# Kernel optimization log

Measured on AMD Instinct MI355X. Metric: run time of the kernel, lower is better.

Reference implementation:

```python
import jax, jax.numpy as jnp
import numpy as np

N, F_IN, HID, E1, E2, P = 100000, 128, 128, 800000, 800000, 200000


def setup_inputs() -> dict:
    key = jax.random.key(0)
    ks = jax.random.split(key, 9)
    x = jax.random.normal(ks[0], (N, F_IN), dtype=jnp.float32)
    edge_index1 = jax.random.randint(ks[1], (2, E1), 0, N)
    edge_index2 = jax.random.randint(ks[2], (2, E2), 0, N)
    edge_weight1 = jax.random.uniform(ks[3], (E1,), dtype=jnp.float32)
    edge_weight2 = jax.random.uniform(ks[4], (E2,), dtype=jnp.float32)
    pos_edge_index = jax.random.randint(ks[5], (2, P), 0, N)
    # parameters (fan-in scaled init)
    W1 = jax.random.normal(ks[6], (F_IN, HID), dtype=jnp.float32) / np.sqrt(F_IN)
    W2 = jax.random.normal(ks[7], (HID, HID), dtype=jnp.float32) / np.sqrt(HID)
    Wlin = jax.random.normal(ks[8], (2, 2 * HID), dtype=jnp.float32) / np.sqrt(2 * HID)  # torch Linear [out,in]
    return {"x": x, "edge_index1": edge_index1, "edge_index2": edge_index2,
            "edge_weight1": edge_weight1, "edge_weight2": edge_weight2,
            "pos_edge_index": pos_edge_index, "W1": W1, "W2": W2, "Wlin": Wlin}


def gcn_conv(x, W, edge_index, edge_weight, num_nodes):
    # GCNConv(add_self_loops=False, normalize=False, bias=False):
    # out[i] = sum_{(j->i) in E} w_e * (x @ W)[j]
    xw = x @ W                                    # [N, H]
    msg = xw[edge_index[0]] * edge_weight[:, None]  # [E, H] gather + scale
    return jax.ops.segment_sum(msg, edge_index[1], num_segments=num_nodes)


def reference(x, edge_index1, edge_index2, edge_weight1, edge_weight2,
              pos_edge_index, W1, W2, Wlin):
    n = x.shape[0]
    h = jax.nn.relu(gcn_conv(x, W1, edge_index1, edge_weight1, n))
    z = gcn_conv(h, W2, edge_index2, edge_weight2, n)          # [N, H]
    pair = jnp.concatenate([z[pos_edge_index[0]], z[pos_edge_index[1]]], axis=1)  # [P, 2H]
    return pair @ Wlin.T                                        # [P, 2]
```

## Files before the change

### kernel.cpp

```cpp
#include <hip/hip_runtime.h>

#define F 128
#define BSH 9
#define BSZ 512
#define NBLKA 256

typedef __bf16 bf16x8 __attribute__((ext_vector_type(8)));
typedef unsigned short ushort8 __attribute__((ext_vector_type(8)));
typedef unsigned short ushort4v __attribute__((ext_vector_type(4)));
typedef float f32x4 __attribute__((ext_vector_type(4)));

static __device__ __forceinline__ unsigned short f2bf(float f) {
    unsigned int u = __float_as_uint(f);
    u += 0x7fffu + ((u >> 16) & 1u);
    return (unsigned short)(u >> 16);
}
static __device__ __forceinline__ void bf2x(unsigned int u, float& lo, float& hi) {
    lo = __uint_as_float(u << 16);
    hi = __uint_as_float(u & 0xffff0000u);
}

#define WPITCH 136

template <int RELU, int INBF>
__global__ __launch_bounds__(256) void gemm128_mfma(const void* __restrict__ Xv,
                                                    const float* __restrict__ W,
                                                    unsigned short* __restrict__ Y,
                                                    int n) {
    __shared__ __align__(16) unsigned short WT[F * WPITCH];
    for (int idx = threadIdx.x; idx < F * F; idx += 256) {
        const int k = idx >> 7, c = idx & 127;
        WT[c * WPITCH + k] = f2bf(W[idx]);
    }
    __syncthreads();

    const int lane = threadIdx.x & 63;
    const int wv = threadIdx.x >> 6;
    const int m15 = lane & 15;
    const int quad = lane >> 4;
    const int rowBase = blockIdx.x * 128 + wv * 32;

    f32x4 acc[2][8];
#pragma unroll
    for (int rt = 0; rt < 2; ++rt)
#pragma unroll
        for (int ct = 0; ct < 8; ++ct) acc[rt][ct] = (f32x4){0.f, 0.f, 0.f, 0.f};

    int rA[2];
    rA[0] = min(rowBase + m15, n - 1);
    rA[1] = min(rowBase + 16 + m15, n - 1);

#pragma unroll
    for (int ks = 0; ks < 4; ++ks) {
        const int k0 = ks * 32 + quad * 8;
        bf16x8 a[2];
#pragma unroll
        for (int rt = 0; rt < 2; ++rt) {
            if (INBF) {
                const unsigned short* Xb = (const unsigned short*)Xv;
                ushort8 u = *(const ushort8*)(Xb + (size_t)rA[rt] * F + k0);
                if (RELU) {
#pragma unroll
                    for (int j = 0; j < 8; ++j) u[j] = (u[j] & 0x8000u) ? 0 : u[j];
                }
                a[rt] = __builtin_bit_cast(bf16x8, u);
            } else {
                const float* Xf = (const float*)Xv;
                const float* p = Xf + (size_t)rA[rt] * F + k0;
                float4 lo = *(const float4*)p;
                float4 hi = *(const float4*)(p + 4);
                if (RELU) {
                    lo.x = fmaxf(lo.x, 0.f); lo.y = fmaxf(lo.y, 0.f);
                    lo.z = fmaxf(lo.z, 0.f); lo.w = fmaxf(lo.w, 0.f);
                    hi.x = fmaxf(hi.x, 0.f); hi.y = fmaxf(hi.y, 0.f);
                    hi.z = fmaxf(hi.z, 0.f); hi.w = fmaxf(hi.w, 0.f);
                }
                ushort8 u;
                u[0] = f2bf(lo.x); u[1] = f2bf(lo.y); u[2] = f2bf(lo.z); u[3] = f2bf(lo.w);
                u[4] = f2bf(hi.x); u[5] = f2bf(hi.y); u[6] = f2bf(hi.z); u[7] = f2bf(hi.w);
                a[rt] = __builtin_bit_cast(bf16x8, u);
            }
        }
#pragma unroll
        for (int ct = 0; ct < 8; ++ct) {
            const int nn = ct * 16 + m15;
            const bf16x8 b = *(const bf16x8*)(WT + nn * WPITCH + k0);
            acc[0][ct] = __builtin_amdgcn_mfma_f32_16x16x32_bf16(a[0], b, acc[0][ct], 0, 0, 0);
            acc[1][ct] = __builtin_amdgcn_mfma_f32_16x16x32_bf16(a[1], b, acc[1][ct], 0, 0, 0);
        }
    }

#pragma unroll
    for (int rt = 0; rt < 2; ++rt)
#pragma unroll
        for (int reg = 0; reg < 4; ++reg) {
            const int row = rowBase + rt * 16 + quad * 4 + reg;
            if (row < n) {
#pragma unroll
                for (int ct = 0; ct < 8; ++ct)
                    Y[(size_t)row * F + ct * 16 + m15] = f2bf(acc[rt][ct][reg]);
            }
        }
}


__global__ __launch_bounds__(256) void binhist(const int* __restrict__ ei,
                                               int* __restrict__ gh, int E, int nbin) {
    __shared__ int h[1024];
    for (int i = threadIdx.x; i < nbin; i += 256) h[i] = 0;
    __syncthreads();
    const int chunk = (E + NBLKA - 1) / NBLKA;
    const int lo = blockIdx.x * chunk;
    const int hi = min(lo + chunk, E);
    for (int e = lo + threadIdx.x; e < hi; e += 256)
        atomicAdd(&h[((unsigned)ei[E + e]) >> BSH], 1);
    __syncthreads();
    for (int i = threadIdx.x; i < nbin; i += 256) gh[i * NBLKA + blockIdx.x] = h[i];
}

__global__ __launch_bounds__(256) void scan_pass1(const int* __restrict__ counts,
                                                  int* __restrict__ bsum, int n) {
    __shared__ int sh[256];
    const int base = blockIdx.x * 1024 + threadIdx.x * 4;
    int s = 0;
#pragma unroll
    for (int j = 0; j < 4; ++j) {
        const int i = base + j;
        if (i < n) s += counts[i];
    }
    sh[threadIdx.x] = s;
    __syncthreads();
    for (int off = 128; off > 0; off >>= 1) {
        if (threadIdx.x < off) sh[threadIdx.x] += sh[threadIdx.x + off];
        __syncthreads();
    }
    if (threadIdx.x == 0) bsum[blockIdx.x] = sh[0];
}

__global__ __launch_bounds__(256) void scan_pass2(int* __restrict__ bsum, int nb) {
    __shared__ int sh[256];
    int v = (threadIdx.x < nb) ? bsum[threadIdx.x] : 0;
    sh[threadIdx.x] = v;
    __syncthreads();
    for (int off = 1; off < 256; off <<= 1) {
        int t = (threadIdx.x >= off) ? sh[threadIdx.x - off] : 0;
        __syncthreads();
        sh[threadIdx.x] += t;
        __syncthreads();
    }
    if (threadIdx.x < nb) bsum[threadIdx.x] = sh[threadIdx.x] - v;
    if (threadIdx.x == nb) bsum[nb] = sh[nb - 1];
}

__global__ __launch_bounds__(256) void scan_pass3(const int* __restrict__ counts,
                                                  const int* __restrict__ bsum,
                                                  int* __restrict__ offs,
                                                  int n, int nb) {
    __shared__ int sh[256];
    const int base = blockIdx.x * 1024 + threadIdx.x * 4;
    int c[4];
    int s = 0;
#pragma unroll
    for (int j = 0; j < 4; ++j) {
        const int i = base + j;
        c[j] = (i < n) ? counts[i] : 0;
        s += c[j];
    }
    int inc = s;
    sh[threadIdx.x] = inc;
    __syncthreads();
    for (int off = 1; off < 256; off <<= 1) {
        int t = (threadIdx.x >= off) ? sh[threadIdx.x - off] : 0;
        __syncthreads();
        sh[threadIdx.x] += t;
        __syncthreads();
    }
    int run = bsum[blockIdx.x] + sh[threadIdx.x] - inc;
#pragma unroll
    for (int j = 0; j < 4; ++j) {
        const int i = base + j;
        if (i < n) offs[i] = run;
        run += c[j];
    }
    if (blockIdx.x == 0 && threadIdx.x == 0) offs[n] = bsum[nb];
}

__global__ __launch_bounds__(256) void binscatter(const int* __restrict__ ei,
                                                  const float* __restrict__ ew,
                                                  const int* __restrict__ ghoffs,
                                                  uint2* __restrict__ Epart,
                                                  int E, int nbin) {
    __shared__ int gbase[1024];
    __shared__ int cur[1024];
    for (int i = threadIdx.x; i < nbin; i += 256) {
        gbase[i] = ghoffs[i * NBLKA + blockIdx.x];
        cur[i] = 0;
    }
    __syncthreads();
    const int chunk = (E + NBLKA - 1) / NBLKA;
    const int lo = blockIdx.x * chunk;
    const int hi = min(lo + chunk, E);
    for (int e = lo + threadIdx.x; e < hi; e += 256) {
        const unsigned int dst = (unsigned int)ei[E + e];
        const unsigned int src = (unsigned int)ei[e];
        const int b = (int)(dst >> BSH);
        const int r = atomicAdd(&cur[b], 1);
        Epart[(size_t)gbase[b] + r] =
            make_uint2(src | ((dst & (BSZ - 1)) << 20), (unsigned)__float_as_int(ew[e]));
    }
}

__global__ __launch_bounds__(512) void sort_bin(const uint2* __restrict__ Epart,
                                                const int* __restrict__ ghoffs,
                                                uint2* __restrict__ Sedge,
                                                int2* __restrict__ ebounds,
                                                int n, int nbin) {
    __shared__ int hist[BSZ], pref[BSZ], cur[BSZ];
    const int bin = blockIdx.x;
    const int tid = threadIdx.x;
    const int base = ghoffs[bin * NBLKA];
    const int end  = ghoffs[(bin + 1) * NBLKA];
    hist[tid] = 0;
    __syncthreads();
    for (int i = base + tid; i < end; i += 512)
        atomicAdd(&hist[Epart[i].x >> 20], 1);
    __syncthreads();
    pref[tid] = hist[tid];
    __syncthreads();
    for (int off = 1; off < BSZ; off <<= 1) {
        int t = (tid >= off) ? pref[tid - off] : 0;
        __syncthreads();
        pref[tid] += t;
        __syncthreads();
    }
    {
        const int inc = pref[tid];
        const int ex = inc - hist[tid];
        cur[tid] = ex;
        const int v = (bin << BSH) + tid;
        if (v < n) ebounds[v] = make_int2(base + ex, base + inc);
    }
    __syncthreads();
    for (int i = base + tid; i < end; i += 512) {
        const uint2 e = Epart[i];
        const int pos = atomicAdd(&cur[e.x >> 20], 1);
        Sedge[(size_t)base + pos] = make_uint2(e.x & 0xFFFFFu, e.y);
    }
}

template <int FUSE_U>
__global__ __launch_bounds__(256) void gather_agg(const unsigned short* __restrict__ XW,
                                                  const int2* __restrict__ ebounds,
                                                  const uint2* __restrict__ Sedge,
                                                  const float* __restrict__ Wlin,
                                                  unsigned short* __restrict__ OUT,
                                                  float4* __restrict__ U, int n) {
    __shared__ float WL[512];
    if (FUSE_U) {
        for (int i = threadIdx.x; i < 512; i += 256) WL[i] = Wlin[i];
        __syncthreads();
    }
    const int l = threadIdx.x & 15;
    const int v = blockIdx.x * 16 + (threadIdx.x >> 4);
    if (v >= n) return;
    float acc[8];
#pragma unroll
    for (int j = 0; j < 8; ++j) acc[j] = 0.f;
    const int2 be = ebounds[v];
    int p = be.x;
    const int e2 = be.y;
    for (; p + 4 <= e2; p += 4) {
        const uint2 s0 = Sedge[p],     s1 = Sedge[p + 1];
        const uint2 s2 = Sedge[p + 2], s3 = Sedge[p + 3];
        const uint4 x0 = ((const uint4*)(XW + (size_t)s0.x * F))[l];
        const uint4 x1 = ((const uint4*)(XW + (size_t)s1.x * F))[l];
        const uint4 x2 = ((const uint4*)(XW + (size_t)s2.x * F))[l];
        const uint4 x3 = ((const uint4*)(XW + (size_t)s3.x * F))[l];
        const float w0 = __int_as_float(s0.y), w1 = __int_as_float(s1.y);
        const float w2 = __int_as_float(s2.y), w3 = __int_as_float(s3.y);
        float a0, a1, a2, a3, a4, a5, a6, a7;
        bf2x(x0.x, a0, a1); bf2x(x0.y, a2, a3); bf2x(x0.z, a4, a5); bf2x(x0.w, a6, a7);
        acc[0] = fmaf(w0, a0, acc[0]); acc[1] = fmaf(w0, a1, acc[1]);
        acc[2] = fmaf(w0, a2, acc[2]); acc[3] = fmaf(w0, a3, acc[3]);
        acc[4] = fmaf(w0, a4, acc[4]); acc[5] = fmaf(w0, a5, acc[5]);
        acc[6] = fmaf(w0, a6, acc[6]); acc[7] = fmaf(w0, a7, acc[7]);
        bf2x(x1.x, a0, a1); bf2x(x1.y, a2, a3); bf2x(x1.z, a4, a5); bf2x(x1.w, a6, a7);
        acc[0] = fmaf(w1, a0, acc[0]); acc[1] = fmaf(w1, a1, acc[1]);
        acc[2] = fmaf(w1, a2, acc[2]); acc[3] = fmaf(w1, a3, acc[3]);
        acc[4] = fmaf(w1, a4, acc[4]); acc[5] = fmaf(w1, a5, acc[5]);
        acc[6] = fmaf(w1, a6, acc[6]); acc[7] = fmaf(w1, a7, acc[7]);
        bf2x(x2.x, a0, a1); bf2x(x2.y, a2, a3); bf2x(x2.z, a4, a5); bf2x(x2.w, a6, a7);
        acc[0] = fmaf(w2, a0, acc[0]); acc[1] = fmaf(w2, a1, acc[1]);
        acc[2] = fmaf(w2, a2, acc[2]); acc[3] = fmaf(w2, a3, acc[3]);
        acc[4] = fmaf(w2, a4, acc[4]); acc[5] = fmaf(w2, a5, acc[5]);
        acc[6] = fmaf(w2, a6, acc[6]); acc[7] = fmaf(w2, a7, acc[7]);
        bf2x(x3.x, a0, a1); bf2x(x3.y, a2, a3); bf2x(x3.z, a4, a5); bf2x(x3.w, a6, a7);
        acc[0] = fmaf(w3, a0, acc[0]); acc[1] = fmaf(w3, a1, acc[1]);
        acc[2] = fmaf(w3, a2, acc[2]); acc[3] = fmaf(w3, a3, acc[3]);
        acc[4] = fmaf(w3, a4, acc[4]); acc[5] = fmaf(w3, a5, acc[5]);
        acc[6] = fmaf(w3, a6, acc[6]); acc[7] = fmaf(w3, a7, acc[7]);
    }
    for (; p < e2; ++p) {
        const uint2 s = Sedge[p];
        const float w = __int_as_float(s.y);
        const uint4 x = ((const uint4*)(XW + (size_t)s.x * F))[l];
        float a0, a1, a2, a3, a4, a5, a6, a7;
        bf2x(x.x, a0, a1); bf2x(x.y, a2, a3); bf2x(x.z, a4, a5); bf2x(x.w, a6, a7);
        acc[0] = fmaf(w, a0, acc[0]); acc[1] = fmaf(w, a1, acc[1]);
        acc[2] = fmaf(w, a2, acc[2]); acc[3] = fmaf(w, a3, acc[3]);
        acc[4] = fmaf(w, a4, acc[4]); acc[5] = fmaf(w, a5, acc[5]);
        acc[6] = fmaf(w, a6, acc[6]); acc[7] = fmaf(w, a7, acc[7]);
    }
    if (!FUSE_U) {
        ushort8 o;
#pragma unroll
        for (int j = 0; j < 8; ++j) o[j] = f2bf(acc[j]);
        *(ushort8*)(OUT + (size_t)v * F + (size_t)l * 8) = o;
    } else {
        const int k = l * 8;
        float s0 = 0.f, s1 = 0.f, s2 = 0.f, s3 = 0.f;
#pragma unroll
        for (int j = 0; j < 8; ++j) {
            s0 = fmaf(acc[j], WL[k + j],       s0);
            s1 = fmaf(acc[j], WL[128 + k + j], s1);
            s2 = fmaf(acc[j], WL[256 + k + j], s2);
            s3 = fmaf(acc[j], WL[384 + k + j], s3);
        }
#pragma unroll
        for (int off = 8; off > 0; off >>= 1) {
            s0 += __shfl_down(s0, off, 16);
            s1 += __shfl_down(s1, off, 16);
            s2 += __shfl_down(s2, off, 16);
            s3 += __shfl_down(s3, off, 16);
        }
        if (l == 0) U[v] = make_float4(s0, s1, s2, s3);
    }
}

__global__ __launch_bounds__(256) void pair_combine(const float4* __restrict__ U,
                                                    const int* __restrict__ pos,
                                                    float* __restrict__ out, int P) {
    const int p = blockIdx.x * 256 + threadIdx.x;
    if (p >= P) return;
    const int a = pos[p];
    const int b = pos[P + p];
    const float4 ua = U[a];
    const float4 ub = U[b];
    *(float2*)(out + (size_t)p * 2) = make_float2(ua.x + ub.y, ua.z + ub.w);
}

extern "C" void kernel_launch(void* const* d_in, const int* in_sizes, int n_in,
                              void* d_out, int out_size, void* d_ws, size_t ws_size,
                              hipStream_t stream) {
    const float* x    = (const float*)d_in[0];
    const int*   ei1  = (const int*)  d_in[1];
    const int*   ei2  = (const int*)  d_in[2];
    const float* ew1  = (const float*)d_in[3];
    const float* ew2  = (const float*)d_in[4];
    const int*   pos  = (const int*)  d_in[5];
    const float* W1   = (const float*)d_in[6];
    const float* W2   = (const float*)d_in[7];
    const float* Wlin = (const float*)d_in[8];
    float* out = (float*)d_out;

    const int N  = in_sizes[0] / F;
    const int E1 = in_sizes[1] / 2;
    const int E2 = in_sizes[2] / 2;
    const int P  = in_sizes[5] / 2;
    const int Emax = E1 > E2 ? E1 : E2;
    const int NBIN = (N + BSZ - 1) >> BSH;
    const int NGH  = NBIN * NBLKA;
    const int NB   = (NGH + 1023) / 1024;

    unsigned short* Abf = (unsigned short*)d_ws;
    unsigned short* Bbf = Abf + (size_t)N * F;
    uintptr_t up  = (uintptr_t)(Bbf + (size_t)N * F);
    up = (up + 15) & ~(uintptr_t)15;
    float4* U       = (float4*)up;
    int2*   ebounds = (int2*)(U + N);
    int*    gh      = (int*)(ebounds + N);
    int*    ghoffs  = gh + NGH;
    int*    bsum    = ghoffs + NGH + 1;
    uintptr_t sp  = (uintptr_t)(bsum + NB + 1);
    sp = (sp + 15) & ~(uintptr_t)15;
    uint2* Epart  = (uint2*)sp;
    uint2* Sedge  = Epart + Emax;

    gemm128_mfma<0, 0><<<(N + 127) / 128, 256, 0, stream>>>(x, W1, Abf, N);

    binhist<<<NBLKA, 256, 0, stream>>>(ei1, gh, E1, NBIN);
    scan_pass1<<<NB, 256, 0, stream>>>(gh, bsum, NGH);
    scan_pass2<<<1, 256, 0, stream>>>(bsum, NB);
    scan_pass3<<<NB, 256, 0, stream>>>(gh, bsum, ghoffs, NGH, NB);
    binscatter<<<NBLKA, 256, 0, stream>>>(ei1, ew1, ghoffs, Epart, E1, NBIN);
    sort_bin<<<NBIN, 512, 0, stream>>>(Epart, ghoffs, Sedge, ebounds, N, NBIN);
    gather_agg<0><<<(N + 15) / 16, 256, 0, stream>>>(Abf, ebounds, Sedge, Wlin, Bbf, U, N);

    gemm128_mfma<1, 1><<<(N + 127) / 128, 256, 0, stream>>>(Bbf, W2, Abf, N);

    binhist<<<NBLKA, 256, 0, stream>>>(ei2, gh, E2, NBIN);
    scan_pass1<<<NB, 256, 0, stream>>>(gh, bsum, NGH);
    scan_pass2<<<1, 256, 0, stream>>>(bsum, NB);
    scan_pass3<<<NB, 256, 0, stream>>>(gh, bsum, ghoffs, NGH, NB);
    binscatter<<<NBLKA, 256, 0, stream>>>(ei2, ew2, ghoffs, Epart, E2, NBIN);
    sort_bin<<<NBIN, 512, 0, stream>>>(Epart, ghoffs, Sedge, ebounds, N, NBIN);
    gather_agg<1><<<(N + 15) / 16, 256, 0, stream>>>(Abf, ebounds, Sedge, Wlin, Bbf, U, N);

    pair_combine<<<(P + 255) / 256, 256, 0, stream>>>(U, pos, out, P);
}
```

Before: 299.1 us.

## Replace scan-based edge binning with atomic per-bin capacity buckets for both layers

```diff
diff --git a/kernel.cpp b/kernel.cpp
--- a/kernel.cpp
+++ b/kernel.cpp
@@ -4,10 +4,11 @@
 #define BSH 9
 #define BSZ 512
 #define NBLKA 256
+#define MAXBIN 256
+#define CSTRIDE 16
 
 typedef __bf16 bf16x8 __attribute__((ext_vector_type(8)));
 typedef unsigned short ushort8 __attribute__((ext_vector_type(8)));
-typedef unsigned short ushort4v __attribute__((ext_vector_type(4)));
 typedef float f32x4 __attribute__((ext_vector_type(4)));
 
 static __device__ __forceinline__ unsigned short f2bf(float f) {
@@ -26,7 +27,13 @@
 __global__ __launch_bounds__(256) void gemm128_mfma(const void* __restrict__ Xv,
                                                     const float* __restrict__ W,
                                                     unsigned short* __restrict__ Y,
-                                                    int n) {
+                                                    int n,
+                                                    int* __restrict__ z1,
+                                                    int* __restrict__ z2, int zn) {
+    if (zn > 0) {
+        if (blockIdx.x == 0) { for (int i = threadIdx.x; i < zn; i += 256) z1[i] = 0; }
+        else if (blockIdx.x == 1) { for (int i = threadIdx.x; i < zn; i += 256) z2[i] = 0; }
+    }
     __shared__ __align__(16) unsigned short WT[F * WPITCH];
     for (int idx = threadIdx.x; idx < F * F; idx += 256) {
         const int k = idx >> 7, c = idx & 127;
@@ -103,127 +110,65 @@
         }
 }
 
-
-__global__ __launch_bounds__(256) void binhist(const int* __restrict__ ei,
-                                               int* __restrict__ gh, int E, int nbin) {
-    __shared__ int h[1024];
+__global__ __launch_bounds__(256) void scatter_both(
+    const int* __restrict__ ei1, const float* __restrict__ ew1,
+    const int* __restrict__ ei2, const float* __restrict__ ew2,
+    int* __restrict__ bc1, int* __restrict__ bc2,
+    uint2* __restrict__ Ep1, uint2* __restrict__ Ep2,
+    int E1, int E2, int nbin, int cap) {
+    __shared__ int h[MAXBIN], base[MAXBIN], cur[MAXBIN];
+    const int layer2 = blockIdx.x >= NBLKA;
+    const int blk = layer2 ? blockIdx.x - NBLKA : blockIdx.x;
+    const int* __restrict__ ei = layer2 ? ei2 : ei1;
+    const float* __restrict__ ew = layer2 ? ew2 : ew1;
+    int* __restrict__ bc = layer2 ? bc2 : bc1;
+    uint2* __restrict__ Ep = layer2 ? Ep2 : Ep1;
+    const int E = layer2 ? E2 : E1;
+
     for (int i = threadIdx.x; i < nbin; i += 256) h[i] = 0;
     __syncthreads();
     const int chunk = (E + NBLKA - 1) / NBLKA;
-    const int lo = blockIdx.x * chunk;
+    const int lo = blk * chunk;
     const int hi = min(lo + chunk, E);
     for (int e = lo + threadIdx.x; e < hi; e += 256)
         atomicAdd(&h[((unsigned)ei[E + e]) >> BSH], 1);
     __syncthreads();
-    for (int i = threadIdx.x; i < nbin; i += 256) gh[i * NBLKA + blockIdx.x] = h[i];
-}
-
-__global__ __launch_bounds__(256) void scan_pass1(const int* __restrict__ counts,
-                                                  int* __restrict__ bsum, int n) {
-    __shared__ int sh[256];
-    const int base = blockIdx.x * 1024 + threadIdx.x * 4;
-    int s = 0;
-#pragma unroll
-    for (int j = 0; j < 4; ++j) {
-        const int i = base + j;
-        if (i < n) s += counts[i];
-    }
-    sh[threadIdx.x] = s;
-    __syncthreads();
-    for (int off = 128; off > 0; off >>= 1) {
-        if (threadIdx.x < off) sh[threadIdx.x] += sh[threadIdx.x + off];
-        __syncthreads();
-    }
-    if (threadIdx.x == 0) bsum[blockIdx.x] = sh[0];
-}
-
-__global__ __launch_bounds__(256) void scan_pass2(int* __restrict__ bsum, int nb) {
-    __shared__ int sh[256];
-    int v = (threadIdx.x < nb) ? bsum[threadIdx.x] : 0;
-    sh[threadIdx.x] = v;
-    __syncthreads();
-    for (int off = 1; off < 256; off <<= 1) {
-        int t = (threadIdx.x >= off) ? sh[threadIdx.x - off] : 0;
-        __syncthreads();
-        sh[threadIdx.x] += t;
-        __syncthreads();
-    }
-    if (threadIdx.x < nb) bsum[threadIdx.x] = sh[threadIdx.x] - v;
-    if (threadIdx.x == nb) bsum[nb] = sh[nb - 1];
-}
-
-__global__ __launch_bounds__(256) void scan_pass3(const int* __restrict__ counts,
-                                                  const int* __restrict__ bsum,
-                                                  int* __restrict__ offs,
-                                                  int n, int nb) {
-    __shared__ int sh[256];
-    const int base = blockIdx.x * 1024 + threadIdx.x * 4;
-    int c[4];
-    int s = 0;
-#pragma unroll
-    for (int j = 0; j < 4; ++j) {
-        const int i = base + j;
-        c[j] = (i < n) ? counts[i] : 0;
-        s += c[j];
-    }
-    int inc = s;
-    sh[threadIdx.x] = inc;
-    __syncthreads();
-    for (int off = 1; off < 256; off <<= 1) {
-        int t = (threadIdx.x >= off) ? sh[threadIdx.x - off] : 0;
-        __syncthreads();
-        sh[threadIdx.x] += t;
-        __syncthreads();
-    }
-    int run = bsum[blockIdx.x] + sh[threadIdx.x] - inc;
-#pragma unroll
-    for (int j = 0; j < 4; ++j) {
-        const int i = base + j;
-        if (i < n) offs[i] = run;
-        run += c[j];
-    }
-    if (blockIdx.x == 0 && threadIdx.x == 0) offs[n] = bsum[nb];
-}
-
-__global__ __launch_bounds__(256) void binscatter(const int* __restrict__ ei,
-                                                  const float* __restrict__ ew,
-                                                  const int* __restrict__ ghoffs,
-                                                  uint2* __restrict__ Epart,
-                                                  int E, int nbin) {
-    __shared__ int gbase[1024];
-    __shared__ int cur[1024];
     for (int i = threadIdx.x; i < nbin; i += 256) {
-        gbase[i] = ghoffs[i * NBLKA + blockIdx.x];
         cur[i] = 0;
-    }
-    __syncthreads();
-    const int chunk = (E + NBLKA - 1) / NBLKA;
-    const int lo = blockIdx.x * chunk;
-    const int hi = min(lo + chunk, E);
+        base[i] = h[i] ? atomicAdd(&bc[i * CSTRIDE], h[i]) : 0;
+    }
+    __syncthreads();
     for (int e = lo + threadIdx.x; e < hi; e += 256) {
         const unsigned int dst = (unsigned int)ei[E + e];
         const unsigned int src = (unsigned int)ei[e];
         const int b = (int)(dst >> BSH);
-        const int r = atomicAdd(&cur[b], 1);
-        Epart[(size_t)gbase[b] + r] =
-            make_uint2(src | ((dst & (BSZ - 1)) << 20), (unsigned)__float_as_int(ew[e]));
-    }
-}
-
-__global__ __launch_bounds__(512) void sort_bin(const uint2* __restrict__ Epart,
-                                                const int* __restrict__ ghoffs,
-                                                uint2* __restrict__ Sedge,
-                                                int2* __restrict__ ebounds,
-                                                int n, int nbin) {
+        const int slot = base[b] + atomicAdd(&cur[b], 1);
+        if (slot < cap)
+            Ep[(size_t)b * cap + slot] =
+                make_uint2(src | ((dst & (BSZ - 1)) << 20), (unsigned)__float_as_int(ew[e]));
+    }
+}
+
+__global__ __launch_bounds__(512) void sort_both(
+    const uint2* __restrict__ Ep1, const uint2* __restrict__ Ep2,
+    const int* __restrict__ bc1, const int* __restrict__ bc2,
+    uint2* __restrict__ Sg1, uint2* __restrict__ Sg2,
+    int2* __restrict__ eb1, int2* __restrict__ eb2,
+    int n, int nbin, int cap) {
     __shared__ int hist[BSZ], pref[BSZ], cur[BSZ];
-    const int bin = blockIdx.x;
+    const int layer2 = blockIdx.x >= nbin;
+    const int bin = layer2 ? blockIdx.x - nbin : blockIdx.x;
+    const uint2* __restrict__ Ep = layer2 ? Ep2 : Ep1;
+    const int* __restrict__ bc = layer2 ? bc2 : bc1;
+    uint2* __restrict__ Sg = layer2 ? Sg2 : Sg1;
+    int2* __restrict__ eb = layer2 ? eb2 : eb1;
     const int tid = threadIdx.x;
-    const int base = ghoffs[bin * NBLKA];
-    const int end  = ghoffs[(bin + 1) * NBLKA];
+    const int base = bin * cap;
+    const int cnt = min(bc[bin * CSTRIDE], cap);
     hist[tid] = 0;
     __syncthreads();
-    for (int i = base + tid; i < end; i += 512)
-        atomicAdd(&hist[Epart[i].x >> 20], 1);
+    for (int i = tid; i < cnt; i += 512)
+        atomicAdd(&hist[Ep[(size_t)base + i].x >> 20], 1);
     __syncthreads();
     pref[tid] = hist[tid];
     __syncthreads();
@@ -238,13 +183,13 @@
         const int ex = inc - hist[tid];
         cur[tid] = ex;
         const int v = (bin << BSH) + tid;
-        if (v < n) ebounds[v] = make_int2(base + ex, base + inc);
-    }
-    __syncthreads();
-    for (int i = base + tid; i < end; i += 512) {
-        const uint2 e = Epart[i];
+        if (v < n) eb[v] = make_int2(base + ex, base + inc);
+    }
+    __syncthreads();
+    for (int i = tid; i < cnt; i += 512) {
+        const uint2 e = Ep[(size_t)base + i];
         const int pos = atomicAdd(&cur[e.x >> 20], 1);
-        Sedge[(size_t)base + pos] = make_uint2(e.x & 0xFFFFFu, e.y);
+        Sg[(size_t)base + pos] = make_uint2(e.x & 0xFFFFFu, e.y);
     }
 }
 
@@ -267,17 +212,21 @@
 #pragma unroll
     for (int j = 0; j < 8; ++j) acc[j] = 0.f;
     const int2 be = ebounds[v];
-    int p = be.x;
     const int e2 = be.y;
-    for (; p + 4 <= e2; p += 4) {
-        const uint2 s0 = Sedge[p],     s1 = Sedge[p + 1];
-        const uint2 s2 = Sedge[p + 2], s3 = Sedge[p + 3];
+    for (int p = be.x; p < e2; p += 4) {
+        const int p1 = min(p + 1, e2 - 1);
+        const int p2 = min(p + 2, e2 - 1);
+        const int p3 = min(p + 3, e2 - 1);
+        const uint2 s0 = Sedge[p],  s1 = Sedge[p1];
+        const uint2 s2 = Sedge[p2], s3 = Sedge[p3];
         const uint4 x0 = ((const uint4*)(XW + (size_t)s0.x * F))[l];
         const uint4 x1 = ((const uint4*)(XW + (size_t)s1.x * F))[l];
         const uint4 x2 = ((const uint4*)(XW + (size_t)s2.x * F))[l];
         const uint4 x3 = ((const uint4*)(XW + (size_t)s3.x * F))[l];
-        const float w0 = __int_as_float(s0.y), w1 = __int_as_float(s1.y);
-        const float w2 = __int_as_float(s2.y), w3 = __int_as_float(s3.y);
+        const float w0 = __int_as_float(s0.y);
+        const float w1 = (p + 1 < e2) ? __int_as_float(s1.y) : 0.f;
+        const float w2 = (p + 2 < e2) ? __int_as_float(s2.y) : 0.f;
+        const float w3 = (p + 3 < e2) ? __int_as_float(s3.y) : 0.f;
         float a0, a1, a2, a3, a4, a5, a6, a7;
         bf2x(x0.x, a0, a1); bf2x(x0.y, a2, a3); bf2x(x0.z, a4, a5); bf2x(x0.w, a6, a7);
         acc[0] = fmaf(w0, a0, acc[0]); acc[1] = fmaf(w0, a1, acc[1]);
@@ -300,17 +249,6 @@
         acc[4] = fmaf(w3, a4, acc[4]); acc[5] = fmaf(w3, a5, acc[5]);
         acc[6] = fmaf(w3, a6, acc[6]); acc[7] = fmaf(w3, a7, acc[7]);
     }
-    for (; p < e2; ++p) {
-        const uint2 s = Sedge[p];
-        const float w = __int_as_float(s.y);
-        const uint4 x = ((const uint4*)(XW + (size_t)s.x * F))[l];
-        float a0, a1, a2, a3, a4, a5, a6, a7;
-        bf2x(x.x, a0, a1); bf2x(x.y, a2, a3); bf2x(x.z, a4, a5); bf2x(x.w, a6, a7);
-        acc[0] = fmaf(w, a0, acc[0]); acc[1] = fmaf(w, a1, acc[1]);
-        acc[2] = fmaf(w, a2, acc[2]); acc[3] = fmaf(w, a3, acc[3]);
-        acc[4] = fmaf(w, a4, acc[4]); acc[5] = fmaf(w, a5, acc[5]);
-        acc[6] = fmaf(w, a6, acc[6]); acc[7] = fmaf(w, a7, acc[7]);
-    }
     if (!FUSE_U) {
         ushort8 o;
 #pragma unroll
@@ -369,42 +307,33 @@
     const int P  = in_sizes[5] / 2;
     const int Emax = E1 > E2 ? E1 : E2;
     const int NBIN = (N + BSZ - 1) >> BSH;
-    const int NGH  = NBIN * NBLKA;
-    const int NB   = (NGH + 1023) / 1024;
+    const int cap  = Emax / NBIN + 512;
 
     unsigned short* Abf = (unsigned short*)d_ws;
     unsigned short* Bbf = Abf + (size_t)N * F;
     uintptr_t up  = (uintptr_t)(Bbf + (size_t)N * F);
     up = (up + 15) & ~(uintptr_t)15;
-    float4* U       = (float4*)up;
-    int2*   ebounds = (int2*)(U + N);
-    int*    gh      = (int*)(ebounds + N);
-    int*    ghoffs  = gh + NGH;
-    int*    bsum    = ghoffs + NGH + 1;
-    uintptr_t sp  = (uintptr_t)(bsum + NB + 1);
+    float4* U     = (float4*)up;
+    int2*   eb1   = (int2*)(U + N);
+    int2*   eb2   = eb1 + N;
+    int*    bc1   = (int*)(eb2 + N);
+    int*    bc2   = bc1 + NBIN * CSTRIDE;
+    uintptr_t sp  = (uintptr_t)(bc2 + NBIN * CSTRIDE);
     sp = (sp + 15) & ~(uintptr_t)15;
-    uint2* Epart  = (uint2*)sp;
-    uint2* Sedge  = Epart + Emax;
-
-    gemm128_mfma<0, 0><<<(N + 127) / 128, 256, 0, stream>>>(x, W1, Abf, N);
-
-    binhist<<<NBLKA, 256, 0, stream>>>(ei1, gh, E1, NBIN);
-    scan_pass1<<<NB, 256, 0, stream>>>(gh, bsum, NGH);
-    scan_pass2<<<1, 256, 0, stream>>>(bsum, NB);
-    scan_pass3<<<NB, 256, 0, stream>>>(gh, bsum, ghoffs, NGH, NB);
-    binscatter<<<NBLKA, 256, 0, stream>>>(ei1, ew1, ghoffs, Epart, E1, NBIN);
-    sort_bin<<<NBIN, 512, 0, stream>>>(Epart, ghoffs, Sedge, ebounds, N, NBIN);
-    gather_agg<0><<<(N + 15) / 16, 256, 0, stream>>>(Abf, ebounds, Sedge, Wlin, Bbf, U, N);
-
-    gemm128_mfma<1, 1><<<(N + 127) / 128, 256, 0, stream>>>(Bbf, W2, Abf, N);
-
-    binhist<<<NBLKA, 256, 0, stream>>>(ei2, gh, E2, NBIN);
-    scan_pass1<<<NB, 256, 0, stream>>>(gh, bsum, NGH);
-    scan_pass2<<<1, 256, 0, stream>>>(bsum, NB);
-    scan_pass3<<<NB, 256, 0, stream>>>(gh, bsum, ghoffs, NGH, NB);
-    binscatter<<<NBLKA, 256, 0, stream>>>(ei2, ew2, ghoffs, Epart, E2, NBIN);
-    sort_bin<<<NBIN, 512, 0, stream>>>(Epart, ghoffs, Sedge, ebounds, N, NBIN);
-    gather_agg<1><<<(N + 15) / 16, 256, 0, stream>>>(Abf, ebounds, Sedge, Wlin, Bbf, U, N);
-
+    uint2* Ep1   = (uint2*)sp;
+    uint2* Sg1   = Ep1 + (size_t)NBIN * cap;
+    uint2* Ep2   = Sg1 + (size_t)NBIN * cap;
+    uint2* Sg2   = Ep2 + (size_t)NBIN * cap;
+
+    gemm128_mfma<0, 0><<<(N + 127) / 128, 256, 0, stream>>>(
+        x, W1, Abf, N, bc1, bc2, NBIN * CSTRIDE);
+    scatter_both<<<2 * NBLKA, 256, 0, stream>>>(
+        ei1, ew1, ei2, ew2, bc1, bc2, Ep1, Ep2, E1, E2, NBIN, cap);
+    sort_both<<<2 * NBIN, 512, 0, stream>>>(
+        Ep1, Ep2, bc1, bc2, Sg1, Sg2, eb1, eb2, N, NBIN, cap);
+    gather_agg<0><<<(N + 15) / 16, 256, 0, stream>>>(Abf, eb1, Sg1, Wlin, Bbf, U, N);
+    gemm128_mfma<1, 1><<<(N + 127) / 128, 256, 0, stream>>>(
+        Bbf, W2, Abf, N, nullptr, nullptr, 0);
+    gather_agg<1><<<(N + 15) / 16, 256, 0, stream>>>(Abf, eb2, Sg2, Wlin, Bbf, U, N);
     pair_combine<<<(P + 255) / 256, 256, 0, stream>>>(U, pos, out, P);
 }
```

Result: faster. 254.2 us (-15.0%).
